# Kernel tuning notes

Measured on AMD Instinct MI355X. Metric: run time of the kernel, lower is better.

## Reference

```python
import jax, jax.numpy as jnp
import numpy as np

MAX_IT = 20
LAMBDA_ROF = 7.0
SIGMA = 1.0 / (7.0 * 0.01)
TAU = 0.01
THETA = 0.5

H, W_DIM = 4096, 4096


def forward_weighted_gradient(x, w):
    # x: (1,H,W), w: (2,H,W) -> (2,H,W)
    x0 = x[0]
    gh = jnp.pad(x0[:, 1:] - x0[:, :-1], ((0, 0), (0, 1)))   # grad[0,:, :-1]
    gv = jnp.pad(x0[1:, :] - x0[:-1, :], ((0, 1), (0, 0)))   # grad[1,:-1,:]
    return jnp.stack([gh, gv], axis=0) * w


def backward_divergence(y):
    # y: (2,H,W) -> (1,H,W)
    yh, yv = y[0], y[1]
    d_h = jnp.concatenate(
        [yh[:, :1], yh[:, 1:-1] - yh[:, :-2], -yh[:, -2:-1]], axis=1)
    d_v = jnp.concatenate(
        [yv[:1, :], yv[1:-1, :] - yv[:-2, :], -yv[-2:-1, :]], axis=0)
    return (d_h + d_v)[None]


def prox_linf_ball(p, r):
    # p - detach(max(p-r,0) - max(-p-r,0))  (clamp treated as data in torch code)
    shrink = jnp.maximum(p - r, 0.0) - jnp.maximum(-p - r, 0.0)
    return p - jax.lax.stop_gradient(shrink)


def setup_inputs() -> dict:
    key = jax.random.key(0)
    k1, _ = jax.random.split(key)
    img_obs = jax.random.uniform(k1, (1, H, W_DIM), dtype=jnp.float32)
    w = jnp.ones((2, H, W_DIM), dtype=jnp.float32)
    return {"img_obs": img_obs, "w": w}


def reference(img_obs, w):
    x0 = img_obs
    x_tilde0 = img_obs
    y0 = jnp.zeros((2,) + img_obs.shape[1:], dtype=img_obs.dtype)

    def step(carry, _):
        x, x_tilde, y = carry
        y = y + SIGMA * forward_weighted_gradient(x_tilde, w)
        y = prox_linf_ball(y, 1.0)
        x_old = x
        x = (x + TAU * backward_divergence(y)
             + LAMBDA_ROF * TAU * img_obs) / (1.0 + LAMBDA_ROF * TAU)
        x_tilde = x + THETA * (x - x_old)
        return (x, x_tilde, y), None

    (x, x_tilde, y), _ = jax.lax.scan(step, (x0, x_tilde0, y0), None, length=MAX_IT)
    return x_tilde
```

## Files before the change

kernel.cpp:

```cpp
#include <hip/hip_runtime.h>

static constexpr int H = 4096;
static constexpr int W = 4096;
static constexpr long N = (long)H * W;

static constexpr int TILE = 64;
static constexpr int HOFF = 12;
static constexpr int R    = TILE + 2*HOFF;
static constexpr int CPR  = R / 8;
static constexpr int PR   = R / 2;
static constexpr int NTASK= PR * CPR;
static constexpr int PSE  = PR * R;
static constexpr int NT   = 512;

static constexpr float SIGMA = 14.285714285714286f;
static constexpr float INVD  = 1.0f / 1.07f;
static constexpr float TIV   = 0.01f / 1.07f;
static constexpr float CF    = 0.07f / 1.07f;

typedef _Float16 half8  __attribute__((ext_vector_type(8)));
typedef _Float16 half4v __attribute__((ext_vector_type(4)));

__device__ __forceinline__ half8 splat8(float f) {
    _Float16 h = (_Float16)f;
    half8 v = {h, h, h, h, h, h, h, h};
    return v;
}
__device__ __forceinline__ half8 clamp8(half8 v) {
    v = __builtin_elementwise_min(v, splat8(1.0f));
    v = __builtin_elementwise_max(v, splat8(-1.0f));
    return v;
}
__device__ __forceinline__ half4v lo4(half8 v) {
    half4v r = {v[0], v[1], v[2], v[3]}; return r;
}
__device__ __forceinline__ half4v hi4(half8 v) {
    half4v r = {v[4], v[5], v[6], v[7]}; return r;
}

__global__ __launch_bounds__(256) void pack_w(
    const float* __restrict__ wg, _Float16* __restrict__ whp, _Float16* __restrict__ wvp)
{
    const long p = ((long)blockIdx.x * 256 + threadIdx.x) * 8;
    const int i = (int)(p >> 12);
    const float4* hp = reinterpret_cast<const float4*>(wg + p);
    float4 a = hp[0], b = hp[1];
    const float4* vp = reinterpret_cast<const float4*>(wg + N + p);
    float4 c = vp[0], d = vp[1];
    half8 wh, wv;
    wh[0]=(_Float16)(SIGMA*a.x); wh[1]=(_Float16)(SIGMA*a.y);
    wh[2]=(_Float16)(SIGMA*a.z); wh[3]=(_Float16)(SIGMA*a.w);
    wh[4]=(_Float16)(SIGMA*b.x); wh[5]=(_Float16)(SIGMA*b.y);
    wh[6]=(_Float16)(SIGMA*b.z); wh[7]=(_Float16)(SIGMA*b.w);
    wv[0]=(_Float16)(SIGMA*c.x); wv[1]=(_Float16)(SIGMA*c.y);
    wv[2]=(_Float16)(SIGMA*c.z); wv[3]=(_Float16)(SIGMA*c.w);
    wv[4]=(_Float16)(SIGMA*d.x); wv[5]=(_Float16)(SIGMA*d.y);
    wv[6]=(_Float16)(SIGMA*d.z); wv[7]=(_Float16)(SIGMA*d.w);
    if ((p & 4095) + 8 == W) wh[7] = (_Float16)0.0f;
    if (i == H - 1) wv = splat8(0.0f);
    *reinterpret_cast<half8*>(whp + p) = wh;
    *reinterpret_cast<half8*>(wvp + p) = wv;
}

template<int PHASE>
__global__ __launch_bounds__(NT, 4) void fused_pd(
    const float* __restrict__ img,
    const _Float16* __restrict__ whp, const _Float16* __restrict__ wvp,
    _Float16* __restrict__ xg, _Float16* __restrict__ yhg, _Float16* __restrict__ yvg,
    float* __restrict__ out)
{
    __shared__ _Float16 lds_s[2 * PSE + 3 * (NTASK + 2)];
    _Float16* __restrict__ xte  = lds_s;
    _Float16* __restrict__ yvo  = lds_s + PSE;
    _Float16* __restrict__ yheA = lds_s + 2 * PSE;
    _Float16* __restrict__ yheB = yheA + (NTASK + 2);
    _Float16* __restrict__ xteo = yheB + (NTASK + 2);

    const int tid = threadIdx.x;
    const bool act = tid < NTASK;
    const int t  = act ? tid : 0;
    const int p  = t / CPR;
    const int j0 = (t - p * CPR) * 8;
    const int be = p * R + j0;
    const int gi0 = blockIdx.y * TILE - HOFF;
    const int gj0 = blockIdx.x * TILE - HOFF;
    const bool interior = (gi0 >= 0) && (gj0 >= 0) && (gi0 + R <= H) && (gj0 + R <= W);

    const half8 kTIV  = splat8(TIV);
    const half8 kINVD = splat8(INVD);
    const half8 k15   = splat8(1.5f);
    const half8 kM05  = splat8(-0.5f);

    half8 wh0, wh1, wv0, wv1;
    half8 ci0, ci1;
    half8 x0, x1;
    half8 xt0r, xt1r;
    half8 yh0, yh1, yv0, yv1;

    auto loadRow = [&](int gi, int gj, half8& whr, half8& wvr, half8& cir,
                       half8& xr, half8& yhr, half8& yvr) {
        if (interior) {
            const long o = (long)gi * W + gj;
            const float4* ip = reinterpret_cast<const float4*>(img + o);
            float4 a = ip[0], b = ip[1];
            float im[8] = {a.x, a.y, a.z, a.w, b.x, b.y, b.z, b.w};
            whr = *reinterpret_cast<const half8*>(whp + o);
            wvr = *reinterpret_cast<const half8*>(wvp + o);
#pragma unroll
            for (int k = 0; k < 8; ++k) cir[k] = (_Float16)(CF * im[k]);
            if (PHASE == 0) {
#pragma unroll
                for (int k = 0; k < 8; ++k) xr[k] = (_Float16)im[k];
                yhr = splat8(0.f); yvr = splat8(0.f);
            } else {
                xr  = *reinterpret_cast<const half8*>(xg  + o);
                yhr = *reinterpret_cast<const half8*>(yhg + o);
                yvr = *reinterpret_cast<const half8*>(yvg + o);
            }
        } else {
            const int gic = min(max(gi, 0), H - 1);
            const bool rowin = (gi >= 0) && (gi < H);
#pragma unroll
            for (int k = 0; k < 8; ++k) {
                const int gjk = gj + k;
                const int gjc = min(max(gjk, 0), W - 1);
                const bool inim = rowin && (gjk >= 0) && (gjk < W);
                const long o = (long)gic * W + gjc;
                const float imf = img[o];
                whr[k] = inim ? whp[o] : (_Float16)0.0f;
                wvr[k] = inim ? wvp[o] : (_Float16)0.0f;
                cir[k] = (_Float16)(CF * imf);
                if (PHASE == 0) {
                    xr[k]  = (_Float16)imf;
                    yhr[k] = (_Float16)0.0f;
                    yvr[k] = (_Float16)0.0f;
                } else {
                    xr[k]  = xg[o];
                    yhr[k] = inim ? yhg[o] : (_Float16)0.0f;
                    yvr[k] = inim ? yvg[o] : (_Float16)0.0f;
                }
            }
        }
    };
    if (act) {
        const int gi = gi0 + 2 * p;
        const int gj = gj0 + j0;
        loadRow(gi,     gj, wh0, wv0, ci0, x0, yh0, yv0);
        loadRow(gi + 1, gj, wh1, wv1, ci1, x1, yh1, yv1);
        if (PHASE == 0) {
            xt0r = x0; xt1r = x1;
            *reinterpret_cast<half8*>(xte + be) = xt0r;
            *reinterpret_cast<half8*>(yvo + be) = splat8(0.f);
            xteo[t] = xt1r[0];
            yheA[1 + t] = (_Float16)0.0f;
            yheB[1 + t] = (_Float16)0.0f;
        } else {
            *reinterpret_cast<half8*>(yvo + be) = yv1;
            yheA[1 + t] = yh0[7];
            yheB[1 + t] = yh1[7];
        }
    }
    if (tid == NT - 1) {
        yheA[0] = (_Float16)0.0f;
        yheB[0] = (_Float16)0.0f;
        xteo[NTASK]     = (_Float16)0.0f;
        xteo[NTASK + 1] = (_Float16)0.0f;
    }
    __syncthreads();

    auto dual_all = [&](bool writes) {
        if (act) {
            _Float16 rt0 = xte[be + 8];
            _Float16 rt1 = xteo[t + 1];
            half8 bv1 = *reinterpret_cast<const half8*>(xte + be + R);
            half8 sh0 = __builtin_shufflevector(xt0r, xt0r, 1, 2, 3, 4, 5, 6, 7, 7);
            sh0[7] = rt0;
            half8 sh1 = __builtin_shufflevector(xt1r, xt1r, 1, 2, 3, 4, 5, 6, 7, 7);
            sh1[7] = rt1;
            yh0 = clamp8((sh0 - xt0r) * wh0 + yh0);
            yv0 = clamp8((xt1r - xt0r) * wv0 + yv0);
            yh1 = clamp8((sh1 - xt1r) * wh1 + yh1);
            yv1 = clamp8((bv1 - xt1r) * wv1 + yv1);
            if (writes) {
                *reinterpret_cast<half8*>(yvo + be) = yv1;
                yheA[1 + t] = yh0[7];
                yheB[1 + t] = yh1[7];
            }
        }
    };
    auto prim_all = [&](bool writes) {
        if (act) {
            _Float16 yl0 = yheA[t];
            _Float16 yl1 = yheB[t];
            half8 yva0 = *reinterpret_cast<const half8*>(yvo + be - R);
            half8 ysh0 = __builtin_shufflevector(yh0, yh0, 0, 0, 1, 2, 3, 4, 5, 6);
            ysh0[0] = yl0;
            half8 ysh1 = __builtin_shufflevector(yh1, yh1, 0, 0, 1, 2, 3, 4, 5, 6);
            ysh1[0] = yl1;
            half8 dv0 = (yh0 - ysh0) + (yv0 - yva0);
            half8 dv1 = (yh1 - ysh1) + (yv1 - yv0);
            half8 tt0 = dv0 * kTIV + ci0;
            half8 xn0 = x0 * kINVD + tt0;
            half8 xtn0 = xn0 * k15 + x0 * kM05;
            x0 = xn0; xt0r = xtn0;
            half8 tt1 = dv1 * kTIV + ci1;
            half8 xn1 = x1 * kINVD + tt1;
            half8 xtn1 = xn1 * k15 + x1 * kM05;
            x1 = xn1; xt1r = xtn1;
            if (writes) {
                *reinterpret_cast<half8*>(xte + be) = xt0r;
                xteo[t] = xt1r[0];
            }
        }
    };

    if (PHASE == 1) {
        prim_all(true);
        __syncthreads();
    }
    const int NIT = (PHASE == 0) ? 10 : 9;
    for (int it = 0; it < NIT; ++it) {
        dual_all(true);
        __syncthreads();
        prim_all(!(PHASE == 1 && it == NIT - 1));
        __syncthreads();
    }
    if (PHASE == 0) {
        dual_all(false);
    }

    if (act && p >= 6 && p < 38 && j0 >= 8 && j0 <= 72) {
        const long g0 = (long)(gi0 + 2 * p) * W + (gj0 + j0);
        const long g1 = g0 + W;
        if (PHASE == 0) {
            if (j0 >= 16 && j0 <= 64) {
                *reinterpret_cast<half8*>(xg  + g0) = x0;
                *reinterpret_cast<half8*>(xg  + g1) = x1;
                *reinterpret_cast<half8*>(yhg + g0) = yh0;
                *reinterpret_cast<half8*>(yhg + g1) = yh1;
                *reinterpret_cast<half8*>(yvg + g0) = yv0;
                *reinterpret_cast<half8*>(yvg + g1) = yv1;
            } else if (j0 == 8) {
                *reinterpret_cast<half4v*>(xg  + g0 + 4) = hi4(x0);
                *reinterpret_cast<half4v*>(xg  + g1 + 4) = hi4(x1);
                *reinterpret_cast<half4v*>(yhg + g0 + 4) = hi4(yh0);
                *reinterpret_cast<half4v*>(yhg + g1 + 4) = hi4(yh1);
                *reinterpret_cast<half4v*>(yvg + g0 + 4) = hi4(yv0);
                *reinterpret_cast<half4v*>(yvg + g1 + 4) = hi4(yv1);
            } else {
                *reinterpret_cast<half4v*>(xg  + g0) = lo4(x0);
                *reinterpret_cast<half4v*>(xg  + g1) = lo4(x1);
                *reinterpret_cast<half4v*>(yhg + g0) = lo4(yh0);
                *reinterpret_cast<half4v*>(yhg + g1) = lo4(yh1);
                *reinterpret_cast<half4v*>(yvg + g0) = lo4(yv0);
                *reinterpret_cast<half4v*>(yvg + g1) = lo4(yv1);
            }
        } else {
            float4 a0 = make_float4((float)xt0r[0], (float)xt0r[1], (float)xt0r[2], (float)xt0r[3]);
            float4 a1 = make_float4((float)xt0r[4], (float)xt0r[5], (float)xt0r[6], (float)xt0r[7]);
            float4 b0 = make_float4((float)xt1r[0], (float)xt1r[1], (float)xt1r[2], (float)xt1r[3]);
            float4 b1 = make_float4((float)xt1r[4], (float)xt1r[5], (float)xt1r[6], (float)xt1r[7]);
            if (j0 >= 16 && j0 <= 64) {
                *reinterpret_cast<float4*>(out + g0)     = a0;
                *reinterpret_cast<float4*>(out + g0 + 4) = a1;
                *reinterpret_cast<float4*>(out + g1)     = b0;
                *reinterpret_cast<float4*>(out + g1 + 4) = b1;
            } else if (j0 == 8) {
                *reinterpret_cast<float4*>(out + g0 + 4) = a1;
                *reinterpret_cast<float4*>(out + g1 + 4) = b1;
            } else {
                *reinterpret_cast<float4*>(out + g0) = a0;
                *reinterpret_cast<float4*>(out + g1) = b0;
            }
        }
    }
}

extern "C" void kernel_launch(void* const* d_in, const int* in_sizes, int n_in,
                              void* d_out, int out_size, void* d_ws, size_t ws_size,
                              hipStream_t stream) {
    const float* img = (const float*)d_in[0];
    const float* wg  = (const float*)d_in[1];
    float* out = (float*)d_out;

    _Float16* ws16 = (_Float16*)d_ws;
    _Float16* whp = ws16;
    _Float16* wvp = ws16 + N;
    _Float16* xg  = ws16 + 2 * N;
    _Float16* yhg = ws16 + 3 * N;
    _Float16* yvg = ws16 + 4 * N;

    pack_w<<<dim3((int)(N / 8 / 256)), dim3(256), 0, stream>>>(wg, whp, wvp);

    dim3 grid(W / TILE, H / TILE);
    fused_pd<0><<<grid, dim3(NT), 0, stream>>>(img, whp, wvp, xg, yhg, yvg, out);
    fused_pd<1><<<grid, dim3(NT), 0, stream>>>(img, whp, wvp, xg, yhg, yvg, out);
}
```

Measured before the change: 342.3 us.

## Use taller 64x128 tiles and pre-pack image into fp16 workspace arrays

```diff
diff --git a/kernel.cpp b/kernel.cpp
--- a/kernel.cpp
+++ b/kernel.cpp
@@ -4,14 +4,16 @@
 static constexpr int W = 4096;
 static constexpr long N = (long)H * W;
 
-static constexpr int TILE = 64;
+static constexpr int TX = 64;
+static constexpr int TY = 128;
 static constexpr int HOFF = 12;
-static constexpr int R    = TILE + 2*HOFF;
-static constexpr int CPR  = R / 8;
-static constexpr int PR   = R / 2;
-static constexpr int NTASK= PR * CPR;
-static constexpr int PSE  = PR * R;
-static constexpr int NT   = 512;
+static constexpr int RX = TX + 2 * HOFF;
+static constexpr int RY = TY + 2 * HOFF;
+static constexpr int CPR = RX / 8;
+static constexpr int PR  = RY / 2;
+static constexpr int NTASK = PR * CPR;
+static constexpr int PSE = PR * RX;
+static constexpr int NT  = 1024;
 
 static constexpr float SIGMA = 14.285714285714286f;
 static constexpr float INVD  = 1.0f / 1.07f;
@@ -38,34 +40,42 @@
     half4v r = {v[4], v[5], v[6], v[7]}; return r;
 }
 
-__global__ __launch_bounds__(256) void pack_w(
-    const float* __restrict__ wg, _Float16* __restrict__ whp, _Float16* __restrict__ wvp)
+__global__ __launch_bounds__(256) void pack_all(
+    const float* __restrict__ img, const float* __restrict__ wg,
+    _Float16* __restrict__ whp, _Float16* __restrict__ wvp,
+    _Float16* __restrict__ cig, _Float16* __restrict__ xgi)
 {
     const long p = ((long)blockIdx.x * 256 + threadIdx.x) * 8;
     const int i = (int)(p >> 12);
+    const float4* ip = reinterpret_cast<const float4*>(img + p);
+    float4 m0 = ip[0], m1 = ip[1];
     const float4* hp = reinterpret_cast<const float4*>(wg + p);
     float4 a = hp[0], b = hp[1];
     const float4* vp = reinterpret_cast<const float4*>(wg + N + p);
     float4 c = vp[0], d = vp[1];
-    half8 wh, wv;
-    wh[0]=(_Float16)(SIGMA*a.x); wh[1]=(_Float16)(SIGMA*a.y);
-    wh[2]=(_Float16)(SIGMA*a.z); wh[3]=(_Float16)(SIGMA*a.w);
-    wh[4]=(_Float16)(SIGMA*b.x); wh[5]=(_Float16)(SIGMA*b.y);
-    wh[6]=(_Float16)(SIGMA*b.z); wh[7]=(_Float16)(SIGMA*b.w);
-    wv[0]=(_Float16)(SIGMA*c.x); wv[1]=(_Float16)(SIGMA*c.y);
-    wv[2]=(_Float16)(SIGMA*c.z); wv[3]=(_Float16)(SIGMA*c.w);
-    wv[4]=(_Float16)(SIGMA*d.x); wv[5]=(_Float16)(SIGMA*d.y);
-    wv[6]=(_Float16)(SIGMA*d.z); wv[7]=(_Float16)(SIGMA*d.w);
-    if ((p & 4095) + 8 == W) wh[7] = (_Float16)0.0f;
-    if (i == H - 1) wv = splat8(0.0f);
-    *reinterpret_cast<half8*>(whp + p) = wh;
-    *reinterpret_cast<half8*>(wvp + p) = wv;
+    float im[8] = {m0.x, m0.y, m0.z, m0.w, m1.x, m1.y, m1.z, m1.w};
+    float wh[8] = {a.x, a.y, a.z, a.w, b.x, b.y, b.z, b.w};
+    float wv[8] = {c.x, c.y, c.z, c.w, d.x, d.y, d.z, d.w};
+    half8 whv, wvv, civ, xv;
+#pragma unroll
+    for (int k = 0; k < 8; ++k) {
+        whv[k] = (_Float16)(SIGMA * wh[k]);
+        wvv[k] = (_Float16)(SIGMA * wv[k]);
+        civ[k] = (_Float16)(CF * im[k]);
+        xv[k]  = (_Float16)im[k];
+    }
+    if ((p & 4095) + 8 == W) whv[7] = (_Float16)0.0f;
+    if (i == H - 1) wvv = splat8(0.0f);
+    *reinterpret_cast<half8*>(whp + p) = whv;
+    *reinterpret_cast<half8*>(wvp + p) = wvv;
+    *reinterpret_cast<half8*>(cig + p) = civ;
+    *reinterpret_cast<half8*>(xgi + p) = xv;
 }
 
 template<int PHASE>
-__global__ __launch_bounds__(NT, 4) void fused_pd(
-    const float* __restrict__ img,
+__global__ __launch_bounds__(NT, 2) void fused_pd(
     const _Float16* __restrict__ whp, const _Float16* __restrict__ wvp,
+    const _Float16* __restrict__ cig, const _Float16* __restrict__ xgi,
     _Float16* __restrict__ xg, _Float16* __restrict__ yhg, _Float16* __restrict__ yvg,
     float* __restrict__ out)
 {
@@ -81,10 +91,10 @@
     const int t  = act ? tid : 0;
     const int p  = t / CPR;
     const int j0 = (t - p * CPR) * 8;
-    const int be = p * R + j0;
-    const int gi0 = blockIdx.y * TILE - HOFF;
-    const int gj0 = blockIdx.x * TILE - HOFF;
-    const bool interior = (gi0 >= 0) && (gj0 >= 0) && (gi0 + R <= H) && (gj0 + R <= W);
+    const int be = p * RX + j0;
+    const int gi0 = blockIdx.y * TY - HOFF;
+    const int gj0 = blockIdx.x * TX - HOFF;
+    const bool interior = (gi0 >= 0) && (gj0 >= 0) && (gi0 + RY <= H) && (gj0 + RX <= W);
 
     const half8 kTIV  = splat8(TIV);
     const half8 kINVD = splat8(INVD);
@@ -101,16 +111,11 @@
                        half8& xr, half8& yhr, half8& yvr) {
         if (interior) {
             const long o = (long)gi * W + gj;
-            const float4* ip = reinterpret_cast<const float4*>(img + o);
-            float4 a = ip[0], b = ip[1];
-            float im[8] = {a.x, a.y, a.z, a.w, b.x, b.y, b.z, b.w};
             whr = *reinterpret_cast<const half8*>(whp + o);
             wvr = *reinterpret_cast<const half8*>(wvp + o);
-#pragma unroll
-            for (int k = 0; k < 8; ++k) cir[k] = (_Float16)(CF * im[k]);
+            cir = *reinterpret_cast<const half8*>(cig + o);
             if (PHASE == 0) {
-#pragma unroll
-                for (int k = 0; k < 8; ++k) xr[k] = (_Float16)im[k];
+                xr  = *reinterpret_cast<const half8*>(xgi + o);
                 yhr = splat8(0.f); yvr = splat8(0.f);
             } else {
                 xr  = *reinterpret_cast<const half8*>(xg  + o);
@@ -126,12 +131,11 @@
                 const int gjc = min(max(gjk, 0), W - 1);
                 const bool inim = rowin && (gjk >= 0) && (gjk < W);
                 const long o = (long)gic * W + gjc;
-                const float imf = img[o];
                 whr[k] = inim ? whp[o] : (_Float16)0.0f;
                 wvr[k] = inim ? wvp[o] : (_Float16)0.0f;
-                cir[k] = (_Float16)(CF * imf);
+                cir[k] = cig[o];
                 if (PHASE == 0) {
-                    xr[k]  = (_Float16)imf;
+                    xr[k]  = xgi[o];
                     yhr[k] = (_Float16)0.0f;
                     yvr[k] = (_Float16)0.0f;
                 } else {
@@ -172,7 +176,7 @@
         if (act) {
             _Float16 rt0 = xte[be + 8];
             _Float16 rt1 = xteo[t + 1];
-            half8 bv1 = *reinterpret_cast<const half8*>(xte + be + R);
+            half8 bv1 = *reinterpret_cast<const half8*>(xte + be + RX);
             half8 sh0 = __builtin_shufflevector(xt0r, xt0r, 1, 2, 3, 4, 5, 6, 7, 7);
             sh0[7] = rt0;
             half8 sh1 = __builtin_shufflevector(xt1r, xt1r, 1, 2, 3, 4, 5, 6, 7, 7);
@@ -192,7 +196,7 @@
         if (act) {
             _Float16 yl0 = yheA[t];
             _Float16 yl1 = yheB[t];
-            half8 yva0 = *reinterpret_cast<const half8*>(yvo + be - R);
+            half8 yva0 = *reinterpret_cast<const half8*>(yvo + be - RX);
             half8 ysh0 = __builtin_shufflevector(yh0, yh0, 0, 0, 1, 2, 3, 4, 5, 6);
             ysh0[0] = yl0;
             half8 ysh1 = __builtin_shufflevector(yh1, yh1, 0, 0, 1, 2, 3, 4, 5, 6);
@@ -229,7 +233,7 @@
         dual_all(false);
     }
 
-    if (act && p >= 6 && p < 38 && j0 >= 8 && j0 <= 72) {
+    if (act && p >= 6 && p < 6 + TY / 2 && j0 >= 8 && j0 <= 72) {
         const long g0 = (long)(gi0 + 2 * p) * W + (gj0 + j0);
         const long g1 = g0 + W;
         if (PHASE == 0) {
@@ -283,16 +287,19 @@
     const float* wg  = (const float*)d_in[1];
     float* out = (float*)d_out;
 
+    _Float16* xgi = (_Float16*)d_out;
+
     _Float16* ws16 = (_Float16*)d_ws;
     _Float16* whp = ws16;
     _Float16* wvp = ws16 + N;
-    _Float16* xg  = ws16 + 2 * N;
-    _Float16* yhg = ws16 + 3 * N;
-    _Float16* yvg = ws16 + 4 * N;
-
-    pack_w<<<dim3((int)(N / 8 / 256)), dim3(256), 0, stream>>>(wg, whp, wvp);
-
-    dim3 grid(W / TILE, H / TILE);
-    fused_pd<0><<<grid, dim3(NT), 0, stream>>>(img, whp, wvp, xg, yhg, yvg, out);
-    fused_pd<1><<<grid, dim3(NT), 0, stream>>>(img, whp, wvp, xg, yhg, yvg, out);
-}
+    _Float16* cig = ws16 + 2 * N;
+    _Float16* xg  = ws16 + 3 * N;
+    _Float16* yhg = ws16 + 4 * N;
+    _Float16* yvg = ws16 + 5 * N;
+
+    pack_all<<<dim3((int)(N / 8 / 256)), dim3(256), 0, stream>>>(img, wg, whp, wvp, cig, xgi);
+
+    dim3 grid(W / TX, H / TY);
+    fused_pd<0><<<grid, dim3(NT), 0, stream>>>(whp, wvp, cig, xgi, xg, yhg, yvg, out);
+    fused_pd<1><<<grid, dim3(NT), 0, stream>>>(whp, wvp, cig, xgi, xg, yhg, yvg, out);
+}
```

Result: slower. 488.2 us (+42.6%).
